# Performance work log

Hardware: AMD Instinct MI355X
Metric: run time of the kernel (lower is better)

## Reference

```python
import jax, jax.numpy as jnp
import numpy as np
import math

EMBED_DIM = 96
NUM_HEADS = 4
HEAD_DIM = EMBED_DIM // NUM_HEADS
RANGE_SIZES = (7, 9, 11)
SCALE = math.sqrt(HEAD_DIM)


def setup_inputs() -> dict:
    key = jax.random.key(0)
    ks = jax.random.split(key, 10)
    B, C, H, W = 2, EMBED_DIM, 64, 64
    s = 1.0 / math.sqrt(C)
    x = jax.random.normal(ks[0], (B, C, H, W), dtype=jnp.float32)
    wq = jax.random.normal(ks[1], (C, C), dtype=jnp.float32) * s
    bq = jax.random.normal(ks[2], (C,), dtype=jnp.float32) * 0.01
    wk = jax.random.normal(ks[3], (C, C), dtype=jnp.float32) * s
    bk = jax.random.normal(ks[4], (C,), dtype=jnp.float32) * 0.01
    wv = jax.random.normal(ks[5], (C, C), dtype=jnp.float32) * s
    bv = jax.random.normal(ks[6], (C,), dtype=jnp.float32) * 0.01
    wo = jax.random.normal(ks[7], (C, C * len(RANGE_SIZES)), dtype=jnp.float32) * (1.0 / math.sqrt(C * len(RANGE_SIZES)))
    bo = jax.random.normal(ks[8], (C,), dtype=jnp.float32) * 0.01
    return {"x": x, "wq": wq, "bq": bq, "wk": wk, "bk": bk,
            "wv": wv, "bv": bv, "wo": wo, "bo": bo}


def _conv1x1(x, w, b):
    # x: (B,Cin,H,W), w: (Cout,Cin) -> (B,Cout,H,W)
    return jnp.einsum('oc,bchw->bohw', w, x) + b[None, :, None, None]


def _unfold_patches(t, k):
    # t: (B,n,d,H,W) -> (B,n,d,k*k,H*W), zero-padded local neighborhoods,
    # kernel offsets row-major to match torch F.unfold ordering.
    B, n, d, H, W = t.shape
    p = k // 2
    tp = jnp.pad(t, ((0, 0), (0, 0), (0, 0), (p, p), (p, p)))
    pats = jnp.stack([tp[..., i:i + H, j:j + W]
                      for i in range(k) for j in range(k)], axis=3)
    return pats.reshape(B, n, d, k * k, H * W)


def reference(x, wq, bq, wk, bk, wv, bv, wo, bo):
    B, C, H, W = x.shape
    n, d = NUM_HEADS, HEAD_DIM
    Q = _conv1x1(x, wq, bq).reshape(B, n, d, H, W)
    K = _conv1x1(x, wk, bk).reshape(B, n, d, H, W)
    V = _conv1x1(x, wv, bv).reshape(B, n, d, H, W)
    Q_flat = Q.reshape(B, n, d, H * W)
    outputs = []
    for k in RANGE_SIZES:
        Kp = _unfold_patches(K, k)  # (B,n,d,kk,HW)
        Vp = _unfold_patches(V, k)
        scores = jnp.einsum('bndh,bndrh->bnrh', Q_flat, Kp) / SCALE
        attn = jax.nn.softmax(scores, axis=2)
        outputs.append(jnp.einsum('bnrh,bndrh->bndh', attn, Vp))
    concat = jnp.concatenate(outputs, axis=2)  # (B,n,d*len(ranges),HW)
    concat = concat.reshape(B, n * d * len(RANGE_SIZES), H, W)
    return _conv1x1(concat, wo, bo)
```

## Files before the change

kernel.cpp:

```cpp
#include <hip/hip_runtime.h>
#include <hip/hip_fp16.h>


#define HW    4096
#define NH    4
#define D     24
#define CC    96
#define C3    288
#define BATCH 2

#define TS    8
#define HALO  5
#define SW    18
#define SPIX  324
#define PSTR  24
#define PBS   29

#define INV_SCALE 0.20412414523193151f

typedef unsigned short u16;
typedef _Float16 h2f __attribute__((ext_vector_type(2)));

__device__ __forceinline__ float fdot2h(unsigned int a, unsigned int b, float c) {
#if __has_builtin(__builtin_amdgcn_fdot2)
    return __builtin_amdgcn_fdot2(__builtin_bit_cast(h2f, a),
                                  __builtin_bit_cast(h2f, b), c, false);
#else
    float2 fa = __half22float2(__builtin_bit_cast(__half2, a));
    float2 fb = __half22float2(__builtin_bit_cast(__half2, b));
    return fmaf(fa.x, fb.x, fmaf(fa.y, fb.y, c));
#endif
}

__device__ __forceinline__ unsigned int packh2(float a, float b) {
    return __builtin_bit_cast(unsigned int, __floats2half2_rn(a, b));
}

__global__ void prep_w(const float* __restrict__ wo, unsigned int* __restrict__ wh) {
    int idx = blockIdx.x * 256 + threadIdx.x;
    if (idx < CC * (C3 / 2)) {
        int o  = idx / (C3 / 2);
        int c2 = idx - o * (C3 / 2);
        wh[idx] = packh2(wo[o * C3 + 2 * c2], wo[o * C3 + 2 * c2 + 1]);
    }
}

__global__ __launch_bounds__(256) void qkv_kernel(
    const float* __restrict__ x,
    const float* __restrict__ wq, const float* __restrict__ bq,
    const float* __restrict__ wk, const float* __restrict__ bk,
    const float* __restrict__ wv, const float* __restrict__ bv,
    u16* __restrict__ Qh, u16* __restrict__ Kh, u16* __restrict__ Vh)
{
    int t   = threadIdx.x;
    int mat = blockIdx.y;
    const float* w    = (mat == 0) ? wq : (mat == 1) ? wk : wv;
    const float* bias = (mat == 0) ? bq : (mat == 1) ? bk : bv;
    u16* dst          = (mat == 0) ? Qh : (mat == 1) ? Kh : Vh;

    int gp = blockIdx.x * 64 + (t & 63);
    int b  = gp >> 12;
    int p  = gp & 4095;
    int o0 = blockIdx.z * 48 + __builtin_amdgcn_readfirstlane(t >> 6) * 12;

    const float* xb = x + (size_t)b * CC * HW + p;

    float acc[12];
    #pragma unroll
    for (int j = 0; j < 12; ++j) acc[j] = bias[o0 + j];

    #pragma unroll
    for (int cb = 0; cb < 6; ++cb) {
        float xc[16];
        #pragma unroll
        for (int i = 0; i < 16; ++i)
            xc[i] = xb[(size_t)(cb * 16 + i) * HW];
        #pragma unroll
        for (int j = 0; j < 12; ++j) {
            const float* wr = w + (o0 + j) * CC + cb * 16;
            #pragma unroll
            for (int i = 0; i < 16; ++i) acc[j] = fmaf(wr[i], xc[i], acc[j]);
        }
    }

    unsigned int u[6];
    #pragma unroll
    for (int i = 0; i < 6; ++i) u[i] = packh2(acc[2 * i], acc[2 * i + 1]);
    uint2* dp = (uint2*)(dst + (size_t)gp * CC + o0);
    dp[0] = make_uint2(u[0], u[1]);
    dp[1] = make_uint2(u[2], u[3]);
    dp[2] = make_uint2(u[4], u[5]);
}

__global__ __launch_bounds__(512) void attn_kernel(
    const u16* __restrict__ Qh, const u16* __restrict__ Kh,
    const u16* __restrict__ Vh, u16* __restrict__ att)
{
    __shared__ __align__(16) char smem_raw[8 * 64 * PBS * 4];
    u16* Ks = (u16*)smem_raw;
    u16* Vs = Ks + SPIX * PSTR;
    float* Pb = (float*)smem_raw;

    int t    = threadIdx.x;
    int wvid = __builtin_amdgcn_readfirstlane(t >> 6);
    int lane = t & 63;
    int bh = blockIdx.z;
    int b  = bh >> 2, h = bh & 3;
    int x0 = blockIdx.x * TS, y0 = blockIdx.y * TS;

    if (t < SPIX) {
        int sp = t;
        int sy = sp / SW, sx = sp - sy * SW;
        int gy = y0 + sy - HALO, gx = x0 + sx - HALO;
        uint4 k0 = make_uint4(0,0,0,0), k1 = k0, k2 = k0;
        uint4 v0 = k0, v1 = k0, v2 = k0;
        if ((unsigned)gy < 64u && (unsigned)gx < 64u) {
            size_t base = ((size_t)(b * HW + gy * 64 + gx) * CC + h * D);
            const uint4* ksrc = (const uint4*)(Kh + base);
            const uint4* vsrc = (const uint4*)(Vh + base);
            k0 = ksrc[0]; k1 = ksrc[1]; k2 = ksrc[2];
            v0 = vsrc[0]; v1 = vsrc[1]; v2 = vsrc[2];
        }
        uint4* kd = (uint4*)(Ks + sp * PSTR);
        uint4* vd = (uint4*)(Vs + sp * PSTR);
        kd[0] = k0; kd[1] = k1; kd[2] = k2;
        vd[0] = v0; vd[1] = v1; vd[2] = v2;
    }
    __syncthreads();

    int ty = lane >> 3, tx = lane & 7;
    int gp = b * HW + (y0 + ty) * 64 + (x0 + tx);

    unsigned int q[12];
    {
        const uint4* qs = (const uint4*)(Qh + (size_t)gp * CC + h * D);
        uint4 a = qs[0], bb = qs[1], c = qs[2];
        q[0]=a.x;  q[1]=a.y;  q[2]=a.z;  q[3]=a.w;
        q[4]=bb.x; q[5]=bb.y; q[6]=bb.z; q[7]=bb.w;
        q[8]=c.x;  q[9]=c.y;  q[10]=c.z; q[11]=c.w;
    }

    float acc[D];
    #pragma unroll
    for (int j = 0; j < D; ++j) acc[j] = 0.f;
    float l  = 0.f;
    int   cp = (ty + HALO) * SW + (tx + HALO);

    auto visit = [&](int di, int dj) {
        int sp = cp + di * SW + dj;
        const uint4* kp = (const uint4*)(Ks + sp * PSTR);
        uint4 k0 = kp[0], k1 = kp[1], k2 = kp[2];
        unsigned int ku[12] = {k0.x,k0.y,k0.z,k0.w, k1.x,k1.y,k1.z,k1.w, k2.x,k2.y,k2.z,k2.w};
        float s = 0.f;
        #pragma unroll
        for (int i = 0; i < 12; ++i) s = fdot2h(ku[i], q[i], s);
        float pw = __expf(s * INV_SCALE);
        l += pw;
        const uint4* vp = (const uint4*)(Vs + sp * PSTR);
        uint4 v0 = vp[0], v1 = vp[1], v2 = vp[2];
        unsigned int vu[12] = {v0.x,v0.y,v0.z,v0.w, v1.x,v1.y,v1.z,v1.w, v2.x,v2.y,v2.z,v2.w};
        #pragma unroll
        for (int i = 0; i < 12; ++i) {
            float2 f = __half22float2(__builtin_bit_cast(__half2, vu[i]));
            acc[2*i]   = fmaf(pw, f.x, acc[2*i]);
            acc[2*i+1] = fmaf(pw, f.y, acc[2*i+1]);
        }
    };

    if (wvid == 0) {
        #pragma unroll
        for (int k = 0; k < 49; k += 4) visit(k / 7 - 3, k % 7 - 3);
    } else if (wvid == 1) {
        #pragma unroll
        for (int k = 1; k < 49; k += 4) visit(k / 7 - 3, k % 7 - 3);
    } else if (wvid == 2) {
        #pragma unroll
        for (int k = 2; k < 49; k += 4) visit(k / 7 - 3, k % 7 - 3);
    } else if (wvid == 3) {
        #pragma unroll
        for (int k = 3; k < 49; k += 4) visit(k / 7 - 3, k % 7 - 3);
    } else if (wvid == 4) {
        #pragma unroll
        for (int dj = -4; dj <= 4; ++dj) visit(-4, dj);
        #pragma unroll
        for (int di = -3; di <= 3; ++di) visit(di, -4);
    } else if (wvid == 5) {
        #pragma unroll
        for (int dj = -4; dj <= 4; ++dj) visit(4, dj);
        #pragma unroll
        for (int di = -3; di <= 3; ++di) visit(di, 4);
    } else if (wvid == 6) {
        #pragma unroll
        for (int dj = -5; dj <= 5; ++dj) visit(-5, dj);
        #pragma unroll
        for (int di = -4; di <= 4; ++di) visit(di, -5);
    } else {
        #pragma unroll
        for (int dj = -5; dj <= 5; ++dj) visit(5, dj);
        #pragma unroll
        for (int di = -4; di <= 4; ++di) visit(di, 5);
    }

    __syncthreads();
    {
        float* pp = Pb + (wvid * 64 + lane) * PBS;
        pp[0] = l;
        #pragma unroll
        for (int i = 0; i < D; ++i) pp[1 + i] = acc[i];
    }
    __syncthreads();

    if (wvid < 3) {
        int N = (wvid == 0) ? 4 : (wvid == 1) ? 6 : 8;
        float L = 0.f;
        float a[D];
        #pragma unroll
        for (int i = 0; i < D; ++i) a[i] = 0.f;
        for (int s = 0; s < N; ++s) {
            const float* pp = Pb + (s * 64 + lane) * PBS;
            L += pp[0];
            #pragma unroll
            for (int i = 0; i < D; ++i) a[i] += pp[1 + i];
        }
        float rl = 1.0f / L;
        unsigned int u[12];
        #pragma unroll
        for (int i = 0; i < 12; ++i)
            u[i] = packh2(a[2 * i] * rl, a[2 * i + 1] * rl);
        uint4* dp = (uint4*)(att + (size_t)gp * C3 + h * 72 + wvid * D);
        dp[0] = make_uint4(u[0], u[1], u[2],  u[3]);
        dp[1] = make_uint4(u[4], u[5], u[6],  u[7]);
        dp[2] = make_uint4(u[8], u[9], u[10], u[11]);
    }
}

#define K3_PAD 65
__global__ __launch_bounds__(256) void proj_kernel(
    const u16* __restrict__ att, const unsigned int* __restrict__ wh,
    const float* __restrict__ bo, float* __restrict__ out)
{
    __shared__ unsigned int ab[(C3 / 2) * K3_PAD];

    int t   = threadIdx.x;
    int gp0 = blockIdx.x * 64;

    const uint4* src = (const uint4*)(att + (size_t)gp0 * C3);
    #pragma unroll
    for (int k = 0; k < 9; ++k) {
        int u   = t + k * 256;
        uint4 v = src[u];
        int px  = u / 36;
        int c20 = (u - px * 36) * 4;
        ab[(c20    ) * K3_PAD + px] = v.x;
        ab[(c20 + 1) * K3_PAD + px] = v.y;
        ab[(c20 + 2) * K3_PAD + px] = v.z;
        ab[(c20 + 3) * K3_PAD + px] = v.w;
    }
    __syncthreads();

    int wvid = __builtin_amdgcn_readfirstlane(t >> 6);
    int o0   = blockIdx.y * 24 + wvid * 6;
    int px   = t & 63;
    int gp   = gp0 + px;
    int b    = gp >> 12, p = gp & 4095;

    float acc[6];
    #pragma unroll
    for (int j = 0; j < 6; ++j) acc[j] = bo[o0 + j];

    #pragma unroll
    for (int cb = 0; cb < 9; ++cb) {
        unsigned int xp[16];
        #pragma unroll
        for (int i = 0; i < 16; ++i) xp[i] = ab[(cb * 16 + i) * K3_PAD + px];
        #pragma unroll
        for (int j = 0; j < 6; ++j) {
            const unsigned int* wr = wh + (o0 + j) * (C3 / 2) + cb * 16;
            #pragma unroll
            for (int i = 0; i < 16; ++i) acc[j] = fdot2h(xp[i], wr[i], acc[j]);
        }
    }

    #pragma unroll
    for (int j = 0; j < 6; ++j)
        out[(size_t)(b * CC + o0 + j) * HW + p] = acc[j];
}

extern "C" void kernel_launch(void* const* d_in, const int* in_sizes, int n_in,
                              void* d_out, int out_size, void* d_ws, size_t ws_size,
                              hipStream_t stream)
{
    const float* x  = (const float*)d_in[0];
    const float* wq = (const float*)d_in[1];
    const float* bq = (const float*)d_in[2];
    const float* wk = (const float*)d_in[3];
    const float* bk = (const float*)d_in[4];
    const float* wv = (const float*)d_in[5];
    const float* bv = (const float*)d_in[6];
    const float* wo = (const float*)d_in[7];
    const float* bo = (const float*)d_in[8];
    float* out = (float*)d_out;

    const size_t NPIX = (size_t)BATCH * HW;
    char* ws = (char*)d_ws;
    u16* Qh  = (u16*)ws;
    u16* Kh  = Qh + NPIX * CC;
    u16* Vh  = Kh + NPIX * CC;
    u16* att = Vh + NPIX * CC;
    unsigned int* wh = (unsigned int*)(att + NPIX * C3);

    prep_w<<<dim3(54), 256, 0, stream>>>(wo, wh);

    qkv_kernel<<<dim3(128, 3, 2), 256, 0, stream>>>(x, wq, bq, wk, bk, wv, bv, Qh, Kh, Vh);

    attn_kernel<<<dim3(8, 8, 8), 512, 0, stream>>>(Qh, Kh, Vh, att);

    proj_kernel<<<dim3(128, 4), 256, 0, stream>>>(att, wh, bo, out);
}
```

Before: 127.7 us.

## Merge weight packing into QKV kernel, roll attention loops, flatten grid

After: 127.4 us. Within noise of the previous version (-0.2%).

```diff
diff --git a/kernel.cpp b/kernel.cpp
--- a/kernel.cpp
+++ b/kernel.cpp
@@ -14,7 +14,7 @@
 #define SW    18
 #define SPIX  324
 #define PSTR  24
-#define PBS   29
+#define PBS   25
 
 #define INV_SCALE 0.20412414523193151f
 
@@ -36,24 +36,29 @@
     return __builtin_bit_cast(unsigned int, __floats2half2_rn(a, b));
 }
 
-__global__ void prep_w(const float* __restrict__ wo, unsigned int* __restrict__ wh) {
-    int idx = blockIdx.x * 256 + threadIdx.x;
-    if (idx < CC * (C3 / 2)) {
-        int o  = idx / (C3 / 2);
-        int c2 = idx - o * (C3 / 2);
-        wh[idx] = packh2(wo[o * C3 + 2 * c2], wo[o * C3 + 2 * c2 + 1]);
-    }
-}
-
-__global__ __launch_bounds__(256) void qkv_kernel(
+__global__ __launch_bounds__(256) void qkv_pack_kernel(
     const float* __restrict__ x,
     const float* __restrict__ wq, const float* __restrict__ bq,
     const float* __restrict__ wk, const float* __restrict__ bk,
     const float* __restrict__ wv, const float* __restrict__ bv,
-    u16* __restrict__ Qh, u16* __restrict__ Kh, u16* __restrict__ Vh)
+    const float* __restrict__ wo,
+    u16* __restrict__ Qh, u16* __restrict__ Kh, u16* __restrict__ Vh,
+    unsigned int* __restrict__ wh)
 {
-    int t   = threadIdx.x;
-    int mat = blockIdx.y;
+    int t  = threadIdx.x;
+    int by = blockIdx.y;
+
+    if (by == 6) {
+        int idx = blockIdx.x * 256 + t;
+        if (blockIdx.x < 54) {
+            int o  = idx / (C3 / 2);
+            int c2 = idx - o * (C3 / 2);
+            wh[idx] = packh2(wo[o * C3 + 2 * c2], wo[o * C3 + 2 * c2 + 1]);
+        }
+        return;
+    }
+
+    int mat = by % 3, z = by / 3;
     const float* w    = (mat == 0) ? wq : (mat == 1) ? wk : wv;
     const float* bias = (mat == 0) ? bq : (mat == 1) ? bk : bv;
     u16* dst          = (mat == 0) ? Qh : (mat == 1) ? Kh : Vh;
@@ -61,7 +66,7 @@
     int gp = blockIdx.x * 64 + (t & 63);
     int b  = gp >> 12;
     int p  = gp & 4095;
-    int o0 = blockIdx.z * 48 + __builtin_amdgcn_readfirstlane(t >> 6) * 12;
+    int o0 = z * 48 + __builtin_amdgcn_readfirstlane(t >> 6) * 12;
 
     const float* xb = x + (size_t)b * CC * HW + p;
 
@@ -69,7 +74,7 @@
     #pragma unroll
     for (int j = 0; j < 12; ++j) acc[j] = bias[o0 + j];
 
-    #pragma unroll
+    #pragma unroll 2
     for (int cb = 0; cb < 6; ++cb) {
         float xc[16];
         #pragma unroll
@@ -96,17 +101,18 @@
     const u16* __restrict__ Qh, const u16* __restrict__ Kh,
     const u16* __restrict__ Vh, u16* __restrict__ att)
 {
-    __shared__ __align__(16) char smem_raw[8 * 64 * PBS * 4];
-    u16* Ks = (u16*)smem_raw;
-    u16* Vs = Ks + SPIX * PSTR;
-    float* Pb = (float*)smem_raw;
+    __shared__ __align__(16) char smem[51200];
+    u16*   Ks = (u16*)smem;
+    u16*   Vs = Ks + SPIX * PSTR;
+    float* Pb = (float*)smem;
 
     int t    = threadIdx.x;
     int wvid = __builtin_amdgcn_readfirstlane(t >> 6);
     int lane = t & 63;
-    int bh = blockIdx.z;
-    int b  = bh >> 2, h = bh & 3;
-    int x0 = blockIdx.x * TS, y0 = blockIdx.y * TS;
+    int blk  = blockIdx.x;
+    int bh   = blk >> 6;
+    int b    = bh >> 2, h = bh & 3;
+    int x0   = (blk & 7) * TS, y0 = ((blk >> 3) & 7) * TS;
 
     if (t < SPIX) {
         int sp = t;
@@ -134,10 +140,10 @@
     unsigned int q[12];
     {
         const uint4* qs = (const uint4*)(Qh + (size_t)gp * CC + h * D);
-        uint4 a = qs[0], bb = qs[1], c = qs[2];
+        uint4 a = qs[0], bb = qs[1], cq = qs[2];
         q[0]=a.x;  q[1]=a.y;  q[2]=a.z;  q[3]=a.w;
         q[4]=bb.x; q[5]=bb.y; q[6]=bb.z; q[7]=bb.w;
-        q[8]=c.x;  q[9]=c.y;  q[10]=c.z; q[11]=c.w;
+        q[8]=cq.x; q[9]=cq.y; q[10]=cq.z; q[11]=cq.w;
     }
 
     float acc[D];
@@ -167,38 +173,24 @@
         }
     };
 
-    if (wvid == 0) {
-        #pragma unroll
-        for (int k = 0; k < 49; k += 4) visit(k / 7 - 3, k % 7 - 3);
-    } else if (wvid == 1) {
-        #pragma unroll
-        for (int k = 1; k < 49; k += 4) visit(k / 7 - 3, k % 7 - 3);
-    } else if (wvid == 2) {
-        #pragma unroll
-        for (int k = 2; k < 49; k += 4) visit(k / 7 - 3, k % 7 - 3);
-    } else if (wvid == 3) {
-        #pragma unroll
-        for (int k = 3; k < 49; k += 4) visit(k / 7 - 3, k % 7 - 3);
-    } else if (wvid == 4) {
-        #pragma unroll
-        for (int dj = -4; dj <= 4; ++dj) visit(-4, dj);
-        #pragma unroll
-        for (int di = -3; di <= 3; ++di) visit(di, -4);
-    } else if (wvid == 5) {
-        #pragma unroll
-        for (int dj = -4; dj <= 4; ++dj) visit(4, dj);
-        #pragma unroll
-        for (int di = -3; di <= 3; ++di) visit(di, 4);
-    } else if (wvid == 6) {
-        #pragma unroll
-        for (int dj = -5; dj <= 5; ++dj) visit(-5, dj);
-        #pragma unroll
-        for (int di = -4; di <= 4; ++di) visit(di, -5);
+    if (wvid < 4) {
+        for (int k = wvid; k < 49; k += 4) {
+            int di = k / 7 - 3;
+            int dj = k - (di + 3) * 7 - 3;
+            visit(di, dj);
+        }
+    } else if (wvid < 6) {
+        for (int j = wvid - 4; j < 32; j += 2) {
+            int di = (j < 9)  ? -4 : (j < 18) ? 4 : (j < 25) ? j - 21 : j - 28;
+            int dj = (j < 9)  ? j - 4 : (j < 18) ? j - 13 : (j < 25) ? -4 : 4;
+            visit(di, dj);
+        }
     } else {
-        #pragma unroll
-        for (int dj = -5; dj <= 5; ++dj) visit(5, dj);
-        #pragma unroll
-        for (int di = -4; di <= 4; ++di) visit(di, 5);
+        for (int j = wvid - 6; j < 40; j += 2) {
+            int di = (j < 11) ? -5 : (j < 22) ? 5 : (j < 31) ? j - 26 : j - 35;
+            int dj = (j < 11) ? j - 5 : (j < 22) ? j - 16 : (j < 31) ? -5 : 5;
+            visit(di, dj);
+        }
     }
 
     __syncthreads();
@@ -245,12 +237,10 @@
     int gp0 = blockIdx.x * 64;
 
     const uint4* src = (const uint4*)(att + (size_t)gp0 * C3);
-    #pragma unroll
-    for (int k = 0; k < 9; ++k) {
-        int u   = t + k * 256;
-        uint4 v = src[u];
-        int px  = u / 36;
-        int c20 = (u - px * 36) * 4;
+    for (int u = t; u < 2304; u += 256) {
+        uint4 v  = src[u];
+        int px   = u / 36;
+        int c20  = (u - px * 36) * 4;
         ab[(c20    ) * K3_PAD + px] = v.x;
         ab[(c20 + 1) * K3_PAD + px] = v.y;
         ab[(c20 + 2) * K3_PAD + px] = v.z;
@@ -259,20 +249,20 @@
     __syncthreads();
 
     int wvid = __builtin_amdgcn_readfirstlane(t >> 6);
+    int lane = t & 63;
     int o0   = blockIdx.y * 24 + wvid * 6;
-    int px   = t & 63;
-    int gp   = gp0 + px;
+    int gp   = gp0 + lane;
     int b    = gp >> 12, p = gp & 4095;
 
     float acc[6];
     #pragma unroll
     for (int j = 0; j < 6; ++j) acc[j] = bo[o0 + j];
 
-    #pragma unroll
+    #pragma unroll 1
     for (int cb = 0; cb < 9; ++cb) {
         unsigned int xp[16];
         #pragma unroll
-        for (int i = 0; i < 16; ++i) xp[i] = ab[(cb * 16 + i) * K3_PAD + px];
+        for (int i = 0; i < 16; ++i) xp[i] = ab[(cb * 16 + i) * K3_PAD + lane];
         #pragma unroll
         for (int j = 0; j < 6; ++j) {
             const unsigned int* wr = wh + (o0 + j) * (C3 / 2) + cb * 16;
@@ -309,11 +299,10 @@
     u16* att = Vh + NPIX * CC;
     unsigned int* wh = (unsigned int*)(att + NPIX * C3);
 
-    prep_w<<<dim3(54), 256, 0, stream>>>(wo, wh);
-
-    qkv_kernel<<<dim3(128, 3, 2), 256, 0, stream>>>(x, wq, bq, wk, bk, wv, bv, Qh, Kh, Vh);
-
-    attn_kernel<<<dim3(8, 8, 8), 512, 0, stream>>>(Qh, Kh, Vh, att);
+    qkv_pack_kernel<<<dim3(128, 7), 256, 0, stream>>>(
+        x, wq, bq, wk, bk, wv, bv, wo, Qh, Kh, Vh, wh);
+
+    attn_kernel<<<dim3(512), 512, 0, stream>>>(Qh, Kh, Vh, att);
 
     proj_kernel<<<dim3(128, 4), 256, 0, stream>>>(att, wh, bo, out);
 }
```
